# Kernel optimization log

Hardware: AMD Instinct MI355X
Metric: run time of the kernel (lower is better)

## Reference

```python
import jax, jax.numpy as jnp
import numpy as np

NUM_TNETS = 8388608
NUM_PINS = 20971520
NUM_NODES = 1048576

def setup_inputs() -> dict:
    key = jax.random.key(0)
    k1, k2, k3 = jax.random.split(key, 3)
    beta = jax.random.uniform(k1, (1,), dtype=jnp.float32)
    tnet_weights = jax.random.uniform(k2, (NUM_TNETS,), dtype=jnp.float32)
    flat_tnet2pin = jax.random.randint(k3, (2 * NUM_TNETS,), 0, NUM_PINS, dtype=jnp.int64)
    pin2node_map = jax.random.randint(jax.random.fold_in(key, 7), (NUM_PINS,), 0, NUM_NODES, dtype=jnp.int64)
    return {
        "beta": beta,
        "tnet_weights": tnet_weights,
        "flat_tnet2pin": flat_tnet2pin,
        "pin2node_map": pin2node_map,
    }

def reference(beta, tnet_weights, flat_tnet2pin, pin2node_map):
    # flat_tnet2pin layout: [src_0, dst_0, src_1, dst_1, ...] (2 pins per timing arc)
    # gather node id for every arc pin: [2*num_tnets]
    node_idx = pin2node_map[flat_tnet2pin]
    # each arc's weight is added at both its source and sink node
    w = jnp.repeat(tnet_weights, 2)  # [w0, w0, w1, w1, ...] matches flat layout
    out = jnp.zeros(NUM_NODES, dtype=jnp.float32).at[node_idx].add(w)
    return out * beta
```

## Files before the change

### kernel.cpp

```cpp
#include <hip/hip_runtime.h>
#include <stdint.h>


#define TILE 4096
#define IPT  16
#define NB1  160
#define SHIFT1 17
#define CAP1 114688
#define TILES_PER_BIN2 28
#define NB2  256
#define SHIFT2 12
#define CAP2 81920
#define ACC_NODES 4096
#define CTRL_BYTES 8192

typedef unsigned long long item_t;
typedef int   int4_ev   __attribute__((ext_vector_type(4)));
typedef float float4_ev __attribute__((ext_vector_type(4)));
typedef unsigned long long ull2_ev __attribute__((ext_vector_type(2)));

__device__ __forceinline__ item_t pack_item(uint32_t key, float w) {
    return (item_t)key | ((item_t)__float_as_uint(w) << 32);
}

template<int NB>
__device__ __forceinline__ void multisplit_flush(
    uint32_t (&key)[IPT], float (&wv)[IPT], int (&bin)[IPT],
    int tile_cnt, int* __restrict__ gcur, item_t* __restrict__ gout, size_t cap)
{
    __shared__ int hist[NB];
    __shared__ int basex[NB];
    __shared__ int gbase[NB];
    __shared__ item_t stage[TILE];
    __shared__ uint8_t binOf[TILE];
    const int t = threadIdx.x;

    for (int b = t; b < NB; b += 256) hist[b] = 0;
    __syncthreads();

    int rank[IPT];
#pragma unroll
    for (int k = 0; k < IPT; ++k)
        rank[k] = (bin[k] >= 0) ? atomicAdd(&hist[bin[k]], 1) : 0;
    __syncthreads();

    if (t < NB) basex[t] = hist[t];
    __syncthreads();
    for (int off = 1; off < NB; off <<= 1) {
        int add = (t < NB && t >= off) ? basex[t - off] : 0;
        __syncthreads();
        if (t < NB) basex[t] += add;
        __syncthreads();
    }
    if (t < NB) basex[t] -= hist[t];
    if (t < NB) gbase[t] = (hist[t] > 0) ? atomicAdd(&gcur[t], hist[t]) : 0;
    __syncthreads();

#pragma unroll
    for (int k = 0; k < IPT; ++k) {
        if (bin[k] >= 0) {
            int pos = basex[bin[k]] + rank[k];
            stage[pos] = pack_item(key[k], wv[k]);
            binOf[pos] = (uint8_t)bin[k];
        }
    }
    __syncthreads();

    for (int j = t; j < tile_cnt; j += 256) {
        int b = binOf[j];
        long long dst = (long long)gbase[b] + (j - basex[b]);
        if (dst >= 0 && dst < (long long)cap)
            __builtin_nontemporal_store(stage[j], &gout[(size_t)b * cap + (size_t)dst]);
    }
    __syncthreads();
}

__global__ __launch_bounds__(256) void k1_partition_pins(
    const int* __restrict__ flat_pins, const float* __restrict__ weights,
    int* __restrict__ cur1, item_t* __restrict__ items1, int total)
{
    const int tileBase = blockIdx.x * TILE;
    const int t = threadIdx.x;
    const int base = tileBase + t * IPT;
    uint32_t key[IPT]; float wv[IPT]; int bin[IPT];

    if (base + IPT <= total) {
        int4_ev   p[4];
        float4_ev w[2];
#pragma unroll
        for (int v = 0; v < 4; ++v)
            p[v] = __builtin_nontemporal_load((const int4_ev*)(flat_pins + base) + v);
#pragma unroll
        for (int v = 0; v < 2; ++v)
            w[v] = __builtin_nontemporal_load((const float4_ev*)(weights + (base >> 1)) + v);
#pragma unroll
        for (int k = 0; k < IPT; ++k) {
            int pin = p[k >> 2][k & 3];
            key[k] = (uint32_t)pin;
            wv[k]  = w[k >> 3][(k >> 1) & 3];
            bin[k] = pin >> SHIFT1;
        }
    } else {
#pragma unroll
        for (int k = 0; k < IPT; ++k) {
            int i = base + k;
            bool ok = i < total;
            int pin = ok ? flat_pins[i] : 0;
            key[k] = (uint32_t)pin;
            wv[k]  = ok ? weights[i >> 1] : 0.f;
            bin[k] = ok ? (pin >> SHIFT1) : -1;
        }
    }
    int cnt = min(TILE, total - tileBase);
    multisplit_flush<NB1>(key, wv, bin, cnt, cur1, items1, (size_t)CAP1);
}

__global__ __launch_bounds__(256) void k2_gather_partition(
    const item_t* __restrict__ items1, const int* __restrict__ cur1,
    const int* __restrict__ pin2node,
    int* __restrict__ cur2, item_t* __restrict__ items2)
{
    const int q = blockIdx.x;
    const int r = q & 7;
    const int s = q >> 3;
    const int bin  = r + 8 * (s / TILES_PER_BIN2);
    const int tile = s % TILES_PER_BIN2;
    const int cnt = min(cur1[bin], (int)CAP1);
    const int tbase = tile * TILE;
    if (tbase >= cnt) return;

    const item_t* src = items1 + (size_t)bin * CAP1;
    const int t = threadIdx.x;
    const int base = tbase + t * IPT;
    uint32_t key[IPT]; float wv[IPT]; int b2[IPT];

    if (base + IPT <= cnt) {
        ull2_ev it[8];
#pragma unroll
        for (int v = 0; v < 8; ++v)
            it[v] = __builtin_nontemporal_load((const ull2_ev*)(src + base) + v);
#pragma unroll
        for (int k = 0; k < IPT; ++k) {
            item_t e = it[k >> 1][k & 1];
            int node = pin2node[(uint32_t)(e & 0xffffffffull)];
            key[k] = (uint32_t)node;
            wv[k]  = __uint_as_float((uint32_t)(e >> 32));
            b2[k]  = node >> SHIFT2;
        }
    } else {
#pragma unroll
        for (int k = 0; k < IPT; ++k) {
            int i = base + k;
            bool ok = i < cnt;
            item_t e = ok ? src[i] : 0ull;
            int node = ok ? pin2node[(uint32_t)(e & 0xffffffffull)] : 0;
            key[k] = (uint32_t)node;
            wv[k]  = __uint_as_float((uint32_t)(e >> 32));
            b2[k]  = ok ? (node >> SHIFT2) : -1;
        }
    }
    int tcnt = min(TILE, cnt - tbase);
    multisplit_flush<NB2>(key, wv, b2, tcnt, cur2, items2, (size_t)CAP2);
}

__global__ __launch_bounds__(1024) void k3_accumulate(
    const item_t* __restrict__ items2, const int* __restrict__ cur2,
    const float* __restrict__ beta, float* __restrict__ out, int num_nodes)
{
    __shared__ float acc[ACC_NODES];
    const int b = blockIdx.x;
    const int t = threadIdx.x;
    for (int i = t; i < ACC_NODES; i += 1024) acc[i] = 0.f;
    __syncthreads();
    const int cnt = min(cur2[b], (int)CAP2);
    const item_t* src = items2 + (size_t)b * CAP2;
    for (int i = t; i < cnt; i += 1024) {
        item_t it = __builtin_nontemporal_load(&src[i]);
        atomicAdd(&acc[(uint32_t)(it & 0xffffffffull) & (ACC_NODES - 1)],
                  __uint_as_float((uint32_t)(it >> 32)));
    }
    __syncthreads();
    const float bt = beta[0];
    const int nodeBase = b << SHIFT2;
    for (int i = t; i < ACC_NODES; i += 1024) {
        int n = nodeBase + i;
        if (n < num_nodes) out[n] = acc[i] * bt;
    }
}

__global__ __launch_bounds__(256) void scatter_device(
    const float* __restrict__ beta, const float* __restrict__ tnet_weights,
    const long long* __restrict__ pin_pairs, const int* __restrict__ pin2node_map,
    float* __restrict__ out, int num_tnets)
{
    int t = blockIdx.x * blockDim.x + threadIdx.x;
    if (t >= num_tnets) return;
    long long pp = pin_pairs[t];
    float w = tnet_weights[t] * beta[0];
    atomicAdd(&out[pin2node_map[(int)(pp & 0xffffffffLL)]], w);
    atomicAdd(&out[pin2node_map[(int)(pp >> 32)]], w);
}

extern "C" void kernel_launch(void* const* d_in, const int* in_sizes, int n_in,
                              void* d_out, int out_size, void* d_ws, size_t ws_size,
                              hipStream_t stream) {
    const float* beta         = (const float*)d_in[0];
    const float* weights      = (const float*)d_in[1];
    const int*   flat_pins    = (const int*)d_in[2];
    const int*   pin2node     = (const int*)d_in[3];
    float* out = (float*)d_out;

    const int num_tnets = in_sizes[1];
    const int total     = in_sizes[2];
    const int num_nodes = out_size;

    const size_t items1Bytes = (size_t)NB1 * CAP1 * sizeof(item_t);
    const size_t items2Bytes = (size_t)NB2 * CAP2 * sizeof(item_t);

    int* cur1 = (int*)d_ws;
    int* cur2 = (int*)((char*)d_ws + 2048);
    const int gridTiles = (total + TILE - 1) / TILE;

    if (ws_size >= CTRL_BYTES + items1Bytes + items2Bytes) {
        item_t* items1 = (item_t*)((char*)d_ws + CTRL_BYTES);
        item_t* items2 = (item_t*)((char*)d_ws + CTRL_BYTES + items1Bytes);
        (void)hipMemsetAsync(d_ws, 0, CTRL_BYTES, stream);
        k1_partition_pins<<<gridTiles, 256, 0, stream>>>(
            flat_pins, weights, cur1, items1, total);
        k2_gather_partition<<<8 * (NB1 / 8) * TILES_PER_BIN2, 256, 0, stream>>>(
            items1, cur1, pin2node, cur2, items2);
        k3_accumulate<<<NB2, 1024, 0, stream>>>(items2, cur2, beta, out, num_nodes);
    } else {
        (void)hipMemsetAsync(d_out, 0, (size_t)out_size * sizeof(float), stream);
        scatter_device<<<(num_tnets + 255) / 256, 256, 0, stream>>>(
            beta, weights, (const long long*)flat_pins, pin2node, out, num_tnets);
    }
}
```

Before: 524.6 us.

## Use 512-thread blocks with wave-shuffle scan and drop binOf staging array

After: 482.7 us. 8.0% less time.

```diff
diff --git a/kernel.cpp b/kernel.cpp
--- a/kernel.cpp
+++ b/kernel.cpp
@@ -3,11 +3,12 @@
 
 
 #define TILE 4096
-#define IPT  16
+#define THREADS 512
+#define IPT  8
 #define NB1  160
 #define SHIFT1 17
 #define CAP1 114688
-#define TILES_PER_BIN2 28
+#define TILES_PER_BIN1 28
 #define NB2  256
 #define SHIFT2 12
 #define CAP2 81920
@@ -23,19 +24,19 @@
     return (item_t)key | ((item_t)__float_as_uint(w) << 32);
 }
 
-template<int NB>
 __device__ __forceinline__ void multisplit_flush(
     uint32_t (&key)[IPT], float (&wv)[IPT], int (&bin)[IPT],
-    int tile_cnt, int* __restrict__ gcur, item_t* __restrict__ gout, size_t cap)
-{
-    __shared__ int hist[NB];
-    __shared__ int basex[NB];
-    __shared__ int gbase[NB];
+    int tile_cnt, int shift,
+    int* __restrict__ gcur, item_t* __restrict__ gout, size_t cap)
+{
+    __shared__ int hist[256];
+    __shared__ int basex[256];
+    __shared__ int gbase[256];
+    __shared__ int wsum[4];
     __shared__ item_t stage[TILE];
-    __shared__ uint8_t binOf[TILE];
-    const int t = threadIdx.x;
-
-    for (int b = t; b < NB; b += 256) hist[b] = 0;
+    const int t = threadIdx.x;
+
+    if (t < 256) hist[t] = 0;
     __syncthreads();
 
     int rank[IPT];
@@ -44,38 +45,42 @@
         rank[k] = (bin[k] >= 0) ? atomicAdd(&hist[bin[k]], 1) : 0;
     __syncthreads();
 
-    if (t < NB) basex[t] = hist[t];
-    __syncthreads();
-    for (int off = 1; off < NB; off <<= 1) {
-        int add = (t < NB && t >= off) ? basex[t - off] : 0;
-        __syncthreads();
-        if (t < NB) basex[t] += add;
-        __syncthreads();
-    }
-    if (t < NB) basex[t] -= hist[t];
-    if (t < NB) gbase[t] = (hist[t] > 0) ? atomicAdd(&gcur[t], hist[t]) : 0;
+    int val = (t < 256) ? hist[t] : 0;
+    int inc = val;
+#pragma unroll
+    for (int d = 1; d < 64; d <<= 1) {
+        int n = __shfl_up(inc, d, 64);
+        if ((t & 63) >= d) inc += n;
+    }
+    if (t < 256 && (t & 63) == 63) wsum[t >> 6] = inc;
+    __syncthreads();
+    if (t < 256) {
+        int w = t >> 6, prefix = 0;
+        if (w > 0) prefix += wsum[0];
+        if (w > 1) prefix += wsum[1];
+        if (w > 2) prefix += wsum[2];
+        basex[t] = prefix + inc - val;
+        gbase[t] = (val > 0) ? atomicAdd(&gcur[t], val) : 0;
+    }
     __syncthreads();
 
 #pragma unroll
     for (int k = 0; k < IPT; ++k) {
-        if (bin[k] >= 0) {
-            int pos = basex[bin[k]] + rank[k];
-            stage[pos] = pack_item(key[k], wv[k]);
-            binOf[pos] = (uint8_t)bin[k];
-        }
-    }
-    __syncthreads();
-
-    for (int j = t; j < tile_cnt; j += 256) {
-        int b = binOf[j];
+        if (bin[k] >= 0)
+            stage[basex[bin[k]] + rank[k]] = pack_item(key[k], wv[k]);
+    }
+    __syncthreads();
+
+    for (int j = t; j < tile_cnt; j += THREADS) {
+        item_t e = stage[j];
+        int b = (int)((uint32_t)(e & 0xffffffffull) >> shift);
         long long dst = (long long)gbase[b] + (j - basex[b]);
         if (dst >= 0 && dst < (long long)cap)
-            __builtin_nontemporal_store(stage[j], &gout[(size_t)b * cap + (size_t)dst]);
-    }
-    __syncthreads();
-}
-
-__global__ __launch_bounds__(256) void k1_partition_pins(
+            __builtin_nontemporal_store(e, &gout[(size_t)b * cap + (size_t)dst]);
+    }
+}
+
+__global__ __launch_bounds__(THREADS, 8) void k1_partition_pins(
     const int* __restrict__ flat_pins, const float* __restrict__ weights,
     int* __restrict__ cur1, item_t* __restrict__ items1, int total)
 {
@@ -85,19 +90,17 @@
     uint32_t key[IPT]; float wv[IPT]; int bin[IPT];
 
     if (base + IPT <= total) {
-        int4_ev   p[4];
-        float4_ev w[2];
-#pragma unroll
-        for (int v = 0; v < 4; ++v)
+        int4_ev   p[2];
+        float4_ev w;
+#pragma unroll
+        for (int v = 0; v < 2; ++v)
             p[v] = __builtin_nontemporal_load((const int4_ev*)(flat_pins + base) + v);
-#pragma unroll
-        for (int v = 0; v < 2; ++v)
-            w[v] = __builtin_nontemporal_load((const float4_ev*)(weights + (base >> 1)) + v);
+        w = __builtin_nontemporal_load((const float4_ev*)(weights + (base >> 1)));
 #pragma unroll
         for (int k = 0; k < IPT; ++k) {
             int pin = p[k >> 2][k & 3];
             key[k] = (uint32_t)pin;
-            wv[k]  = w[k >> 3][(k >> 1) & 3];
+            wv[k]  = w[(k >> 1) & 3];
             bin[k] = pin >> SHIFT1;
         }
     } else {
@@ -112,10 +115,10 @@
         }
     }
     int cnt = min(TILE, total - tileBase);
-    multisplit_flush<NB1>(key, wv, bin, cnt, cur1, items1, (size_t)CAP1);
-}
-
-__global__ __launch_bounds__(256) void k2_gather_partition(
+    multisplit_flush(key, wv, bin, cnt, SHIFT1, cur1, items1, (size_t)CAP1);
+}
+
+__global__ __launch_bounds__(THREADS, 8) void k2_gather_partition(
     const item_t* __restrict__ items1, const int* __restrict__ cur1,
     const int* __restrict__ pin2node,
     int* __restrict__ cur2, item_t* __restrict__ items2)
@@ -123,8 +126,8 @@
     const int q = blockIdx.x;
     const int r = q & 7;
     const int s = q >> 3;
-    const int bin  = r + 8 * (s / TILES_PER_BIN2);
-    const int tile = s % TILES_PER_BIN2;
+    const int bin  = r + 8 * (s / TILES_PER_BIN1);
+    const int tile = s % TILES_PER_BIN1;
     const int cnt = min(cur1[bin], (int)CAP1);
     const int tbase = tile * TILE;
     if (tbase >= cnt) return;
@@ -135,9 +138,9 @@
     uint32_t key[IPT]; float wv[IPT]; int b2[IPT];
 
     if (base + IPT <= cnt) {
-        ull2_ev it[8];
-#pragma unroll
-        for (int v = 0; v < 8; ++v)
+        ull2_ev it[4];
+#pragma unroll
+        for (int v = 0; v < 4; ++v)
             it[v] = __builtin_nontemporal_load((const ull2_ev*)(src + base) + v);
 #pragma unroll
         for (int k = 0; k < IPT; ++k) {
@@ -160,7 +163,7 @@
         }
     }
     int tcnt = min(TILE, cnt - tbase);
-    multisplit_flush<NB2>(key, wv, b2, tcnt, cur2, items2, (size_t)CAP2);
+    multisplit_flush(key, wv, b2, tcnt, SHIFT2, cur2, items2, (size_t)CAP2);
 }
 
 __global__ __launch_bounds__(1024) void k3_accumulate(
@@ -225,9 +228,9 @@
         item_t* items1 = (item_t*)((char*)d_ws + CTRL_BYTES);
         item_t* items2 = (item_t*)((char*)d_ws + CTRL_BYTES + items1Bytes);
         (void)hipMemsetAsync(d_ws, 0, CTRL_BYTES, stream);
-        k1_partition_pins<<<gridTiles, 256, 0, stream>>>(
+        k1_partition_pins<<<gridTiles, THREADS, 0, stream>>>(
             flat_pins, weights, cur1, items1, total);
-        k2_gather_partition<<<8 * (NB1 / 8) * TILES_PER_BIN2, 256, 0, stream>>>(
+        k2_gather_partition<<<NB1 * TILES_PER_BIN1, THREADS, 0, stream>>>(
             items1, cur1, pin2node, cur2, items2);
         k3_accumulate<<<NB2, 1024, 0, stream>>>(items2, cur2, beta, out, num_nodes);
     } else {
```
